# Performance work log

Measured on AMD Instinct MI355X. Metric: run time of the kernel, lower is better.

Reference implementation:

```python
import jax, jax.numpy as jnp
import numpy as np

EMBED = 768
HEADS = 12
D_K = EMBED // HEADS  # 64


def setup_inputs() -> dict:
    key = jax.random.key(0)
    ks = jax.random.split(key, 9)
    w_scale = EMBED ** -0.5
    inp = {
        "x": jax.random.normal(ks[0], (128, 256, 1, EMBED), dtype=jnp.float32),
        "Wq": jax.random.normal(ks[1], (EMBED, EMBED), dtype=jnp.float32) * w_scale,
        "bq": jax.random.normal(ks[2], (EMBED,), dtype=jnp.float32) * 0.02,
        "Wk": jax.random.normal(ks[3], (EMBED, EMBED), dtype=jnp.float32) * w_scale,
        "bk": jax.random.normal(ks[4], (EMBED,), dtype=jnp.float32) * 0.02,
        "Wv": jax.random.normal(ks[5], (EMBED, EMBED), dtype=jnp.float32) * w_scale,
        "bv": jax.random.normal(ks[6], (EMBED,), dtype=jnp.float32) * 0.02,
        "Wo": jax.random.normal(ks[7], (EMBED, EMBED), dtype=jnp.float32) * w_scale,
        "bo": jax.random.normal(ks[8], (EMBED,), dtype=jnp.float32) * 0.02,
    }
    return inp


def reference(x, Wq, bq, Wk, bk, Wv, bv, Wo, bo):
    # x: (n_rows r, n_cols i/j, batch n, embed)
    R, C, B, E = x.shape
    H, Dk = HEADS, D_K
    # tied-row scaling: d_k^{-1/2} / sqrt(n_rows)
    scaling = (Dk ** -0.5) / np.sqrt(R).astype(np.float32)

    q = (x @ Wq.T + bq).reshape(R, C, B, H, Dk) * scaling
    k = (x @ Wk.T + bk).reshape(R, C, B, H, Dk)
    v = (x @ Wv.T + bv).reshape(R, C, B, H, Dk)

    # scores summed over rows r and head dim d -> (h, n, i, j)
    scores = jnp.einsum('rinhd,rjnhd->hnij', q, k)
    probs = jax.nn.softmax(scores, axis=-1)  # dropout p=0 -> identity

    # shared attention applied per row
    c = jnp.einsum('hnij,rjnhd->rinhd', probs, v).reshape(R, C, B, E)
    out = c @ Wo.T + bo
    return (out, probs)
```

## Files before the change

### kernel.cpp

```cpp
#include <hip/hip_runtime.h>
#include <math.h>

typedef short bf16x8 __attribute__((ext_vector_type(8)));
typedef float f32x4 __attribute__((ext_vector_type(4)));
typedef unsigned short ushort8 __attribute__((ext_vector_type(8)));
typedef unsigned short ushort4v __attribute__((ext_vector_type(4)));

constexpr int R = 128, Cc = 256, E = 768, H = 12;
constexpr int M = R * Cc;
constexpr size_t TOK = (size_t)M * E;

__device__ __forceinline__ unsigned short f2b(float f) {
  unsigned int u = __float_as_uint(f);
  u += 0x7fff + ((u >> 16) & 1);
  return (unsigned short)(u >> 16);
}

__device__ __forceinline__ void ldst16(const unsigned short* g, unsigned short* l) {
  __builtin_amdgcn_global_load_lds(
      (const __attribute__((address_space(1))) unsigned int*)g,
      (__attribute__((address_space(3))) unsigned int*)l, 16, 0, 0);
}

__global__ __launch_bounds__(256) void cvt_bf16(const float* __restrict__ in,
                                                unsigned short* __restrict__ out,
                                                int n8) {
  int i = blockIdx.x * 256 + threadIdx.x;
  if (i >= n8) return;
  const float4* p = (const float4*)in;
  float4 a = p[2 * i], b = p[2 * i + 1];
  ushort8 o;
  o[0] = f2b(a.x); o[1] = f2b(a.y); o[2] = f2b(a.z); o[3] = f2b(a.w);
  o[4] = f2b(b.x); o[5] = f2b(b.y); o[6] = f2b(b.z); o[7] = f2b(b.w);
  ((ushort8*)out)[i] = o;
}

__device__ __forceinline__ void gemm128(const unsigned short* __restrict__ A, int lda,
                                        const unsigned short* __restrict__ B, int ldb,
                                        int K, unsigned short* As, unsigned short* Bs,
                                        int wv, int ln, int wm, int wn,
                                        f32x4 (&acc)[4][4]) {
  const int srow = ln >> 3, scol = (ln & 7) * 8;
  for (int k0 = 0; k0 < K; k0 += 64) {
    __syncthreads();
#pragma unroll
    for (int t = 0; t < 4; ++t) {
      const int ch = wv * 4 + t;
      const int row = ch * 8 + srow;
      ldst16(A + (size_t)row * lda + k0 + scol, As + ch * 512 + ln * 8);
      ldst16(B + (size_t)row * ldb + k0 + scol, Bs + ch * 512 + ln * 8);
    }
    __syncthreads();
#pragma unroll
    for (int dk = 0; dk < 2; ++dk) {
      bf16x8 a[4], b[4];
#pragma unroll
      for (int i = 0; i < 4; ++i)
        a[i] = *(const bf16x8*)(As + (wm + i * 16 + (ln & 15)) * 64 + dk * 32 + (ln >> 4) * 8);
#pragma unroll
      for (int j = 0; j < 4; ++j)
        b[j] = *(const bf16x8*)(Bs + (wn + j * 16 + (ln & 15)) * 64 + dk * 32 + (ln >> 4) * 8);
#pragma unroll
      for (int i = 0; i < 4; ++i)
#pragma unroll
        for (int j = 0; j < 4; ++j)
          acc[i][j] = __builtin_amdgcn_mfma_f32_16x16x32_bf16(a[i], b[j], acc[i][j], 0, 0, 0);
    }
  }
}

__global__ __launch_bounds__(256) void qkv_proj(
    const unsigned short* __restrict__ A, const unsigned short* __restrict__ B,
    const float* __restrict__ bq, const float* __restrict__ bk,
    const float* __restrict__ bv, unsigned short* __restrict__ q2,
    unsigned short* __restrict__ k2, unsigned short* __restrict__ v3, float scaling) {
  __shared__ unsigned short As[128 * 64];
  __shared__ unsigned short Bs[128 * 64];
  const int tid = threadIdx.x, wv = tid >> 6, ln = tid & 63;
  const unsigned p = blockIdx.x + blockIdx.y * 18;
  const unsigned l = (p & 7) * 576 + (p >> 3);
  const int bx = l % 18, by = l / 18;
  const int n0 = bx * 128, m0 = by * 128;
  const int wm = (wv & 1) * 64, wn = (wv >> 1) * 64;
  f32x4 acc[4][4] = {};
  gemm128(A + (size_t)m0 * 768, 768, B + (size_t)n0 * 768, 768, 768,
          As, Bs, wv, ln, wm, wn, acc);

  const int region = bx / 6;
  const float* bias = region == 0 ? bq : (region == 1 ? bk : bv);
  const float sc = region == 0 ? scaling : 1.0f;
  const int nq0 = n0 - region * 768;
#pragma unroll
  for (int j = 0; j < 4; ++j) {
    const int np = nq0 + wn + j * 16 + (ln & 15);
    const int h = np >> 6, d = np & 63;
    const float bn = bias[np];
#pragma unroll
    for (int i = 0; i < 4; ++i) {
      const int mb = m0 + wm + i * 16 + (ln >> 4) * 4;
      if (region < 2) {
        unsigned short* dst = region == 0 ? q2 : k2;
#pragma unroll
        for (int r = 0; r < 4; ++r) {
          const int m = mb + r;
          const int ic = m & 255, rr = m >> 8;
          dst[(size_t)h * 2097152 + (size_t)ic * 8192 + rr * 64 + d] =
              f2b((acc[i][j][r] + bn) * sc);
        }
      } else {
        const int jc = mb & 255, rr = mb >> 8;
        ushort4v o;
#pragma unroll
        for (int r = 0; r < 4; ++r) o[r] = f2b(acc[i][j][r] + bn);
        *(ushort4v*)(v3 + (size_t)h * 2097152 + ((size_t)rr * 64 + d) * 256 + jc) = o;
      }
    }
  }
}

__global__ __launch_bounds__(256) void qk_gemm(const unsigned short* __restrict__ q2,
                                               const unsigned short* __restrict__ k2,
                                               float* __restrict__ Sp) {
  __shared__ unsigned short As[128 * 64];
  __shared__ unsigned short Bs[128 * 64];
  const int tid = threadIdx.x, wv = tid >> 6, ln = tid & 63;
  const int i0 = (blockIdx.x & 1) * 128, j0 = (blockIdx.x >> 1) * 128;
  const int h = blockIdx.y, kc = blockIdx.z;
  const int wm = (wv & 1) * 64, wn = (wv >> 1) * 64;
  f32x4 acc[4][4] = {};
  const unsigned short* Ap = q2 + (size_t)h * 2097152 + (size_t)i0 * 8192 + kc * 1024;
  const unsigned short* Bp = k2 + (size_t)h * 2097152 + (size_t)j0 * 8192 + kc * 1024;
  gemm128(Ap, 8192, Bp, 8192, 1024, As, Bs, wv, ln, wm, wn, acc);
  float* out = Sp + ((size_t)kc * H + h) * 65536;
#pragma unroll
  for (int j = 0; j < 4; ++j) {
    const int jj = j0 + wn + j * 16 + (ln & 15);
#pragma unroll
    for (int i = 0; i < 4; ++i)
#pragma unroll
      for (int r = 0; r < 4; ++r) {
        const int ii = i0 + wm + i * 16 + (ln >> 4) * 4 + r;
        out[(size_t)ii * 256 + jj] = acc[i][j][r];
      }
  }
}

__global__ __launch_bounds__(256) void softmax_k(const float* __restrict__ Sp,
                                                 float* __restrict__ P,
                                                 unsigned short* __restrict__ Pb) {
  const int row = blockIdx.x, j = threadIdx.x;
  const size_t stride = (size_t)H * Cc * Cc;
  const size_t base = (size_t)row * Cc + j;
  float s = 0.f;
#pragma unroll
  for (int c = 0; c < 8; ++c) s += Sp[base + c * stride];
  float m = s;
#pragma unroll
  for (int o = 32; o > 0; o >>= 1) m = fmaxf(m, __shfl_xor(m, o));
  __shared__ float sm[4], ss[4];
  const int wid = j >> 6, lane = j & 63;
  if (lane == 0) sm[wid] = m;
  __syncthreads();
  m = fmaxf(fmaxf(sm[0], sm[1]), fmaxf(sm[2], sm[3]));
  float e = expf(s - m);
  float t = e;
#pragma unroll
  for (int o = 32; o > 0; o >>= 1) t += __shfl_xor(t, o);
  if (lane == 0) ss[wid] = t;
  __syncthreads();
  t = ss[0] + ss[1] + ss[2] + ss[3];
  const float p = e / t;
  P[base] = p;
  Pb[base] = f2b(p);
}

__global__ __launch_bounds__(256) void pv_gemm(const unsigned short* __restrict__ P,
                                               const unsigned short* __restrict__ V,
                                               unsigned short* __restrict__ Co) {
  __shared__ unsigned short As[128 * 64];
  __shared__ unsigned short Bs[128 * 64];
  const int tid = threadIdx.x, wv = tid >> 6, ln = tid & 63;
  const unsigned p = blockIdx.x + blockIdx.y * 128;
  const unsigned l = (p & 7) * 192 + (p >> 3);
  const int bx = l & 127, h = l >> 7;
  const int i0 = (bx & 1) * 128, n0 = (bx >> 1) * 128;
  const int wm = (wv & 1) * 64, wn = (wv >> 1) * 64;
  f32x4 acc[4][4] = {};
  const unsigned short* Ap = P + (size_t)h * 65536 + (size_t)i0 * 256;
  const unsigned short* Bp = V + (size_t)h * 2097152 + (size_t)n0 * 256;
  gemm128(Ap, 256, Bp, 256, 256, As, Bs, wv, ln, wm, wn, acc);
#pragma unroll
  for (int j = 0; j < 4; ++j) {
    const int n = n0 + wn + j * 16 + (ln & 15);
    const int rr = n >> 6, d = n & 63;
#pragma unroll
    for (int i = 0; i < 4; ++i)
#pragma unroll
      for (int r = 0; r < 4; ++r) {
        const int ii = i0 + wm + i * 16 + (ln >> 4) * 4 + r;
        Co[((size_t)rr * 256 + ii) * 768 + h * 64 + d] = f2b(acc[i][j][r]);
      }
  }
}

__global__ __launch_bounds__(256) void o_proj(const unsigned short* __restrict__ A,
                                              const unsigned short* __restrict__ B,
                                              const float* __restrict__ bias,
                                              float* __restrict__ Y) {
  __shared__ unsigned short As[128 * 64];
  __shared__ unsigned short Bs[128 * 64];
  const int tid = threadIdx.x, wv = tid >> 6, ln = tid & 63;
  const unsigned p = blockIdx.x + blockIdx.y * 6;
  const unsigned l = (p & 7) * 192 + (p >> 3);
  const int bx = l % 6, by = l / 6;
  const int n0 = bx * 128, m0 = by * 128;
  const int wm = (wv & 1) * 64, wn = (wv >> 1) * 64;
  f32x4 acc[4][4] = {};
  gemm128(A + (size_t)m0 * 768, 768, B + (size_t)n0 * 768, 768, 768,
          As, Bs, wv, ln, wm, wn, acc);
#pragma unroll
  for (int j = 0; j < 4; ++j) {
    const int n = n0 + wn + j * 16 + (ln & 15);
    const float bn = bias[n];
#pragma unroll
    for (int i = 0; i < 4; ++i)
#pragma unroll
      for (int r = 0; r < 4; ++r) {
        const int m = m0 + wm + i * 16 + (ln >> 4) * 4 + r;
        Y[(size_t)m * 768 + n] = acc[i][j][r] + bn;
      }
  }
}

extern "C" void kernel_launch(void* const* d_in, const int* in_sizes, int n_in,
                              void* d_out, int out_size, void* d_ws, size_t ws_size,
                              hipStream_t stream) {
  const float* x  = (const float*)d_in[0];
  const float* Wq = (const float*)d_in[1];
  const float* bq = (const float*)d_in[2];
  const float* Wk = (const float*)d_in[3];
  const float* bk = (const float*)d_in[4];
  const float* Wv = (const float*)d_in[5];
  const float* bv = (const float*)d_in[6];
  const float* Wo = (const float*)d_in[7];
  const float* bo = (const float*)d_in[8];
  float* out = (float*)d_out;
  float* probs = out + TOK;

  char* ws = (char*)d_ws;
  unsigned short* x_bf  = (unsigned short*)(ws);
  unsigned short* q2    = (unsigned short*)(ws + 50331648);
  unsigned short* k2    = (unsigned short*)(ws + 100663296);
  unsigned short* v3    = (unsigned short*)(ws + 150994944);
  unsigned short* Wq_bf = (unsigned short*)(ws + 201326592);
  unsigned short* Wk_bf = Wq_bf + 589824;
  unsigned short* Wv_bf = Wk_bf + 589824;
  unsigned short* Wo_bf = Wv_bf + 589824;
  float* S_part         = (float*)(ws);
  unsigned short* P_bf  = (unsigned short*)(ws + 25165824);
  unsigned short* c_bf  = q2;

  const float scaling = 0.125f / sqrtf(128.f);

  cvt_bf16<<<12288, 256, 0, stream>>>(x, x_bf, 3145728);
  cvt_bf16<<<288, 256, 0, stream>>>(Wq, Wq_bf, 73728);
  cvt_bf16<<<288, 256, 0, stream>>>(Wk, Wk_bf, 73728);
  cvt_bf16<<<288, 256, 0, stream>>>(Wv, Wv_bf, 73728);
  cvt_bf16<<<288, 256, 0, stream>>>(Wo, Wo_bf, 73728);

  qkv_proj<<<dim3(18, 256), 256, 0, stream>>>(x_bf, Wq_bf, bq, bk, bv,
                                              q2, k2, v3, scaling);

  qk_gemm<<<dim3(4, H, 8), 256, 0, stream>>>(q2, k2, S_part);
  softmax_k<<<H * Cc, 256, 0, stream>>>(S_part, probs, P_bf);
  pv_gemm<<<dim3(128, H), 256, 0, stream>>>(P_bf, v3, c_bf);

  o_proj<<<dim3(6, 256), 256, 0, stream>>>(c_bf, Wo_bf, bo, out);
}
```

Measured before the change: 553.3 us.

## Double-buffer LDS tiles in shared GEMM and XOR-swizzle LDS layout

The shared 128x128 GEMM mainloop now uses two LDS buffers, issuing the global-to-LDS load of the next K-tile before computing on the current one, with one barrier per iteration instead of two. The LDS column index is also XOR-swizzled by row, on both the store and the fragment reads, to cut bank conflicts. This doubles LDS per block to 64KB, which may lower occupancy. It also relies on the async global_load_lds being complete at the single barrier without an explicit vmcnt wait.

```diff
diff --git a/kernel.cpp b/kernel.cpp
--- a/kernel.cpp
+++ b/kernel.cpp
@@ -35,37 +35,53 @@
   ((ushort8*)out)[i] = o;
 }
 
+__device__ __forceinline__ void stage64(const unsigned short* __restrict__ A, int lda,
+                                        const unsigned short* __restrict__ B, int ldb,
+                                        int k0, unsigned short* As, unsigned short* Bs,
+                                        int wv, int ln, int srow, int scol) {
+#pragma unroll
+  for (int t = 0; t < 4; ++t) {
+    const int ch = wv * 4 + t;
+    const int row = ch * 8 + srow;
+    ldst16(A + (size_t)row * lda + k0 + scol, As + ch * 512 + ln * 8);
+    ldst16(B + (size_t)row * ldb + k0 + scol, Bs + ch * 512 + ln * 8);
+  }
+}
+
 __device__ __forceinline__ void gemm128(const unsigned short* __restrict__ A, int lda,
                                         const unsigned short* __restrict__ B, int ldb,
                                         int K, unsigned short* As, unsigned short* Bs,
                                         int wv, int ln, int wm, int wn,
                                         f32x4 (&acc)[4][4]) {
-  const int srow = ln >> 3, scol = (ln & 7) * 8;
+  const int srow = ln >> 3;
+  const int scol = ((ln & 7) ^ srow) * 8;
+  stage64(A, lda, B, ldb, 0, As, Bs, wv, ln, srow, scol);
+  __syncthreads();
+  int cur = 0;
   for (int k0 = 0; k0 < K; k0 += 64) {
-    __syncthreads();
-#pragma unroll
-    for (int t = 0; t < 4; ++t) {
-      const int ch = wv * 4 + t;
-      const int row = ch * 8 + srow;
-      ldst16(A + (size_t)row * lda + k0 + scol, As + ch * 512 + ln * 8);
-      ldst16(B + (size_t)row * ldb + k0 + scol, Bs + ch * 512 + ln * 8);
-    }
-    __syncthreads();
+    if (k0 + 64 < K)
+      stage64(A, lda, B, ldb, k0 + 64, As + (cur ^ 1) * 8192, Bs + (cur ^ 1) * 8192,
+              wv, ln, srow, scol);
+    const unsigned short* Ab = As + cur * 8192;
+    const unsigned short* Bb = Bs + cur * 8192;
 #pragma unroll
     for (int dk = 0; dk < 2; ++dk) {
+      const int rc = ((dk * 4 + (ln >> 4)) ^ (ln & 7)) * 8;
       bf16x8 a[4], b[4];
 #pragma unroll
       for (int i = 0; i < 4; ++i)
-        a[i] = *(const bf16x8*)(As + (wm + i * 16 + (ln & 15)) * 64 + dk * 32 + (ln >> 4) * 8);
+        a[i] = *(const bf16x8*)(Ab + (wm + i * 16 + (ln & 15)) * 64 + rc);
 #pragma unroll
       for (int j = 0; j < 4; ++j)
-        b[j] = *(const bf16x8*)(Bs + (wn + j * 16 + (ln & 15)) * 64 + dk * 32 + (ln >> 4) * 8);
+        b[j] = *(const bf16x8*)(Bb + (wn + j * 16 + (ln & 15)) * 64 + rc);
 #pragma unroll
       for (int i = 0; i < 4; ++i)
 #pragma unroll
         for (int j = 0; j < 4; ++j)
           acc[i][j] = __builtin_amdgcn_mfma_f32_16x16x32_bf16(a[i], b[j], acc[i][j], 0, 0, 0);
     }
+    __syncthreads();
+    cur ^= 1;
   }
 }
 
@@ -74,8 +90,8 @@
     const float* __restrict__ bq, const float* __restrict__ bk,
     const float* __restrict__ bv, unsigned short* __restrict__ q2,
     unsigned short* __restrict__ k2, unsigned short* __restrict__ v3, float scaling) {
-  __shared__ unsigned short As[128 * 64];
-  __shared__ unsigned short Bs[128 * 64];
+  __shared__ unsigned short As[2 * 128 * 64];
+  __shared__ unsigned short Bs[2 * 128 * 64];
   const int tid = threadIdx.x, wv = tid >> 6, ln = tid & 63;
   const unsigned p = blockIdx.x + blockIdx.y * 18;
   const unsigned l = (p & 7) * 576 + (p >> 3);
@@ -121,8 +137,8 @@
 __global__ __launch_bounds__(256) void qk_gemm(const unsigned short* __restrict__ q2,
                                                const unsigned short* __restrict__ k2,
                                                float* __restrict__ Sp) {
-  __shared__ unsigned short As[128 * 64];
-  __shared__ unsigned short Bs[128 * 64];
+  __shared__ unsigned short As[2 * 128 * 64];
+  __shared__ unsigned short Bs[2 * 128 * 64];
   const int tid = threadIdx.x, wv = tid >> 6, ln = tid & 63;
   const int i0 = (blockIdx.x & 1) * 128, j0 = (blockIdx.x >> 1) * 128;
   const int h = blockIdx.y, kc = blockIdx.z;
@@ -177,8 +193,8 @@
 __global__ __launch_bounds__(256) void pv_gemm(const unsigned short* __restrict__ P,
                                                const unsigned short* __restrict__ V,
                                                unsigned short* __restrict__ Co) {
-  __shared__ unsigned short As[128 * 64];
-  __shared__ unsigned short Bs[128 * 64];
+  __shared__ unsigned short As[2 * 128 * 64];
+  __shared__ unsigned short Bs[2 * 128 * 64];
   const int tid = threadIdx.x, wv = tid >> 6, ln = tid & 63;
   const unsigned p = blockIdx.x + blockIdx.y * 128;
   const unsigned l = (p & 7) * 192 + (p >> 3);
@@ -207,8 +223,8 @@
                                               const unsigned short* __restrict__ B,
                                               const float* __restrict__ bias,
                                               float* __restrict__ Y) {
-  __shared__ unsigned short As[128 * 64];
-  __shared__ unsigned short Bs[128 * 64];
+  __shared__ unsigned short As[2 * 128 * 64];
+  __shared__ unsigned short Bs[2 * 128 * 64];
   const int tid = threadIdx.x, wv = tid >> 6, ln = tid & 63;
   const unsigned p = blockIdx.x + blockIdx.y * 6;
   const unsigned l = (p & 7) * 192 + (p >> 3);
```

Measured after the change: 537.5 us. 1.03x faster.
